# Kernel optimization log

Hardware: AMD Instinct MI355X
Metric: run time of the kernel (lower is better)

Reference implementation:

```python
import jax, jax.numpy as jnp
import numpy as np

EPS = 1e-6
B, S, D, H = 2, 1024, 1024, 16
HD = D // H


def setup_inputs() -> dict:
    key = jax.random.key(0)
    ks = jax.random.split(key, 16)
    def n(k, shape, s=1.0):
        return jax.random.normal(k, shape, dtype=jnp.float32) * s
    def u(k, shape):
        # positive scales in [0.01, 0.11)
        return jax.random.uniform(k, shape, dtype=jnp.float32) * 0.1 + 0.01
    return {
        'q_loc': n(ks[0], (B, S, D)), 'q_scale': u(ks[1], (B, S, D)),
        'k_loc': n(ks[2], (B, S, D)), 'k_scale': u(ks[3], (B, S, D)),
        'v_loc': n(ks[4], (B, S, D)), 'v_scale': u(ks[5], (B, S, D)),
        'Wq': n(ks[6], (D, D), 0.02), 'bq': n(ks[7], (D,), 0.02),
        'Wk': n(ks[8], (D, D), 0.02), 'bk': n(ks[9], (D,), 0.02),
        'Wv': n(ks[10], (D, D), 0.02), 'bv': n(ks[11], (D,), 0.02),
        'Wo': n(ks[12], (D, D), 0.02), 'bo': n(ks[13], (D,), 0.02),
        'tau': jnp.ones((), dtype=jnp.float32),
    }


def _affine(loc, scale, W, b):
    # GaussianDiag.affine: mean -> x@W^T+b ; var -> var @ (W^2)^T (diag-Gaussian linear push-through)
    new_loc = loc @ W.T + b
    new_scale = jnp.sqrt((scale * scale) @ (W * W).T)
    return new_loc, new_scale


def _split(x):  # [B,S,D] -> [B,H,S,HD]
    b, s, d = x.shape
    return x.reshape(b, s, H, d // H).transpose(0, 2, 1, 3)


def _merge(x):  # [B,H,S,HD] -> [B,S,D]
    b, h, s, hd = x.shape
    return x.transpose(0, 2, 1, 3).reshape(b, s, h * hd)


def reference(q_loc, q_scale, k_loc, k_scale, v_loc, v_scale,
              Wq, bq, Wk, bk, Wv, bv, Wo, bo, tau):
    # projections (mean and variance paths)
    qm, qs = _affine(q_loc, q_scale, Wq, bq)
    km, ks_ = _affine(k_loc, k_scale, Wk, bk)
    vm, vs = _affine(v_loc, v_scale, Wv, bv)

    qmu, kmu, vmu = _split(qm), _split(km), _split(vm)       # [B,H,S,HD]
    vvar = (_split(vs) + EPS) ** 2                           # GaussianDiag(split(loc), log(split(scale)+eps))

    # bilinear_moment: mean path matmul, variance path is constant 0.1 (+eps through log-sqrt wrap)
    score_mu = jnp.einsum('bhsd,bhtd->bhst', qmu, kmu)       # [B,H,S,S]
    score_var = jnp.float32(0.1) + EPS

    # scale by sqrt(head_dim) / head_dim
    s_mu = score_mu / np.float32(np.sqrt(HD))
    s_var = score_var / HD + EPS

    # temperature
    l_mu = s_mu / tau
    l_var = s_var / (tau * tau) + EPS                        # scalar (traced)

    # softmax_via_samples: softmax of mean, constant scale 0.01 -> var 1e-4
    top_mu = jax.nn.softmax(l_mu, axis=-1)
    top_var = jnp.float32(1e-4)

    # softmax_logit_normal (probit approximation + delta-method variance)
    adj = l_mu / jnp.sqrt(1.0 + (jnp.pi / 8.0) * l_var)
    rest_mu = jax.nn.softmax(adj, axis=-1)
    rest_var = rest_mu * (1.0 - rest_mu) * l_var

    # combine_top_rest: add means and variances (+eps through wrap)
    attn_mu = top_mu + rest_mu
    attn_var = top_var + rest_var + EPS

    # linear_combination: attn.mean @ V.mean ; attn.var @ V.var
    y_mu = jnp.einsum('bhst,bhtd->bhsd', attn_mu, vmu)
    y_var = jnp.einsum('bhst,bhtd->bhsd', attn_var, vvar)
    y_scale = jnp.sqrt(y_var + EPS)

    out_loc_pre = _merge(y_mu)
    out_scale_pre = _merge(y_scale) + EPS
    out_loc, out_scale = _affine(out_loc_pre, out_scale_pre, Wo, bo)
    return out_loc, out_scale
```

## Files before the change

### kernel.cpp

```cpp
#include <hip/hip_runtime.h>

typedef unsigned short ushort_t;
typedef __attribute__((ext_vector_type(4))) short sh4;
typedef __attribute__((ext_vector_type(8))) short short8;
typedef __attribute__((ext_vector_type(4))) float floatx4;

#define EPS 1e-6f

static __device__ __forceinline__ float b2f(ushort_t u) {
  unsigned int x = ((unsigned int)u) << 16;
  return __builtin_bit_cast(float, x);
}
static __device__ __forceinline__ ushort_t f2b(float f) {
  unsigned int u = __builtin_bit_cast(unsigned int, f);
  u = (u + 0x7FFFu + ((u >> 16) & 1u)) >> 16;
  return (ushort_t)u;
}
static __device__ __forceinline__ bool tau_is_f32(const void* taup) {
  return ((const ushort_t*)taup)[0] == 0;
}
static __device__ __forceinline__ float read_tau(const void* taup) {
  return tau_is_f32(taup) ? ((const float*)taup)[0] : b2f(((const ushort_t*)taup)[0]);
}

__global__ __launch_bounds__(256) void convert_kernel(
    const void* s0, const void* s1, const void* s2, const void* s3,
    const void* s4, const void* s5, const void* s6,
    ushort_t* __restrict__ dst, const void* taup)
{
  if (!tau_is_f32(taup)) return;
  int seg = blockIdx.y;
  const void* src; int size; int off;
  switch (seg) {
    case 0: src = s0; size = 2097152; off = 0;       break;
    case 1: src = s1; size = 2097152; off = 2097152; break;
    case 2: src = s2; size = 2097152; off = 4194304; break;
    case 3: src = s3; size = 1048576; off = 6291456; break;
    case 4: src = s4; size = 1048576; off = 7340032; break;
    case 5: src = s5; size = 1048576; off = 8388608; break;
    default: src = s6; size = 1048576; off = 9437184; break;
  }
  int i = (blockIdx.x * 256 + threadIdx.x) * 4;
  if (i >= size) return;
  ushort_t* d = dst + off + i;
  float4 v = ((const float4*)src)[i >> 2];
  d[0] = f2b(v.x); d[1] = f2b(v.y); d[2] = f2b(v.z); d[3] = f2b(v.w);
}

__global__ __launch_bounds__(256) void gemm_proj(
    const ushort_t* cA0, const ushort_t* cA1, const ushort_t* cA2,
    const ushort_t* cB0, const ushort_t* cB1, const ushort_t* cB2,
    const void* oA0, const void* oA1, const void* oA2,
    const void* oB0, const void* oB1, const void* oB2,
    const void* b0, const void* b1, const void* b2p,
    ushort_t* C0, ushort_t* C1, ushort_t* vtp,
    const void* taup)
{
  const int K = 1024, N = 1024;
  int z = blockIdx.z;
  bool f32io = tau_is_f32(taup);
  const ushort_t* A = f32io ? ((z == 0) ? cA0 : ((z == 1) ? cA1 : cA2))
                            : (const ushort_t*)((z == 0) ? oA0 : ((z == 1) ? oA1 : oA2));
  const ushort_t* B = f32io ? ((z == 0) ? cB0 : ((z == 1) ? cB1 : cB2))
                            : (const ushort_t*)((z == 0) ? oB0 : ((z == 1) ? oB1 : oB2));
  const void* bias  = (z == 0) ? b0 : ((z == 1) ? b1 : b2p);
  ushort_t* C       = (z == 0) ? C0 : C1;

  __shared__ __align__(16) ushort_t a_s[128 * 72];
  __shared__ __align__(16) ushort_t b_s[128 * 72];

  int tid = threadIdx.x;
  int lane = tid & 63, w = tid >> 6;
  int quad = lane >> 4, l16 = lane & 15;
  int m0 = blockIdx.y * 128, n0 = blockIdx.x * 128;
  int wm = (w & 1) * 64, wn = (w >> 1) * 64;

  floatx4 acc[4][4] = {};
  int srow = tid >> 3;
  int scol = (tid & 7) * 8;

  short8 pa[4], pb[4];
#pragma unroll
  for (int p = 0; p < 4; p++) {
    pa[p] = *(const short8*)(A + (size_t)(m0 + srow + p * 32) * K + scol);
    pb[p] = *(const short8*)(B + (size_t)(n0 + srow + p * 32) * K + scol);
  }

  for (int k0 = 0; k0 < K; k0 += 64) {
    __syncthreads();
#pragma unroll
    for (int p = 0; p < 4; p++) {
      *(short8*)(&a_s[(srow + p * 32) * 72 + scol]) = pa[p];
      *(short8*)(&b_s[(srow + p * 32) * 72 + scol]) = pb[p];
    }
    __syncthreads();
    if (k0 + 64 < K) {
#pragma unroll
      for (int p = 0; p < 4; p++) {
        pa[p] = *(const short8*)(A + (size_t)(m0 + srow + p * 32) * K + k0 + 64 + scol);
        pb[p] = *(const short8*)(B + (size_t)(n0 + srow + p * 32) * K + k0 + 64 + scol);
      }
    }
#pragma unroll
    for (int half = 0; half < 2; half++) {
      short8 af[4], bf[4];
#pragma unroll
      for (int i = 0; i < 4; i++)
        af[i] = *(short8*)(&a_s[(wm + i * 16 + l16) * 72 + half * 32 + quad * 8]);
#pragma unroll
      for (int j = 0; j < 4; j++)
        bf[j] = *(short8*)(&b_s[(wn + j * 16 + l16) * 72 + half * 32 + quad * 8]);
      __builtin_amdgcn_s_setprio(1);
#pragma unroll
      for (int i = 0; i < 4; i++)
#pragma unroll
        for (int j = 0; j < 4; j++)
          acc[i][j] = __builtin_amdgcn_mfma_f32_16x16x32_bf16(af[i], bf[j], acc[i][j], 0, 0, 0);
      __builtin_amdgcn_s_setprio(0);
    }
  }

  float bvv[4];
#pragma unroll
  for (int j = 0; j < 4; j++) {
    int n = n0 + wn + j * 16 + l16;
    bvv[j] = f32io ? ((const float*)bias)[n] : b2f(((const ushort_t*)bias)[n]);
  }
  if (z == 2) {
#pragma unroll
    for (int i = 0; i < 4; i++)
#pragma unroll
      for (int j = 0; j < 4; j++) {
        int n = n0 + wn + j * 16 + l16;
        int mrow = m0 + wm + i * 16 + quad * 4;
        int bb = mrow >> 10, s = mrow & 1023;
        sh4 pk4;
#pragma unroll
        for (int r = 0; r < 4; r++) pk4[r] = (short)f2b(acc[i][j][r] + bvv[j]);
        *(sh4*)(vtp + ((size_t)((bb * 16 + (n >> 6)) * 64 + (n & 63))) * 1024 + s) = pk4;
      }
  } else {
#pragma unroll
    for (int i = 0; i < 4; i++)
#pragma unroll
      for (int j = 0; j < 4; j++) {
        int n = n0 + wn + j * 16 + l16;
#pragma unroll
        for (int r = 0; r < 4; r++) {
          int m = m0 + wm + i * 16 + quad * 4 + r;
          C[(size_t)m * N + n] = f2b(acc[i][j][r] + bvv[j]);
        }
      }
  }
}

__global__ __launch_bounds__(256) void gemm_out64(
    const ushort_t* __restrict__ Abf,
    const void* __restrict__ Bv,
    const void* __restrict__ biasv,
    const ushort_t* __restrict__ Bc,
    const float* __restrict__ rsc,
    void* __restrict__ C,
    const void* taup)
{
  const int K = 1024, N = 1024;
  bool f32io = tau_is_f32(taup);
  const ushort_t* B = f32io ? Bc : (const ushort_t*)Bv;

  __shared__ __align__(16) ushort_t a_s[64 * 72];
  __shared__ __align__(16) ushort_t b_s[64 * 72];

  int tid = threadIdx.x;
  int lane = tid & 63, w = tid >> 6;
  int quad = lane >> 4, l16 = lane & 15;
  int m0 = blockIdx.y * 64, n0 = blockIdx.x * 64;
  int wm = (w & 1) * 32, wn = (w >> 1) * 32;

  floatx4 acc[2][2] = {};
  int srow = tid >> 3;
  int scol = (tid & 7) * 8;

  short8 pa[2], pb[2];
#pragma unroll
  for (int p = 0; p < 2; p++) {
    pa[p] = *(const short8*)(Abf + (size_t)(m0 + srow + p * 32) * K + scol);
    pb[p] = *(const short8*)(B + (size_t)(n0 + srow + p * 32) * K + scol);
  }

  for (int k0 = 0; k0 < K; k0 += 64) {
    __syncthreads();
#pragma unroll
    for (int p = 0; p < 2; p++) {
      *(short8*)(&a_s[(srow + p * 32) * 72 + scol]) = pa[p];
      *(short8*)(&b_s[(srow + p * 32) * 72 + scol]) = pb[p];
    }
    __syncthreads();
    if (k0 + 64 < K) {
#pragma unroll
      for (int p = 0; p < 2; p++) {
        pa[p] = *(const short8*)(Abf + (size_t)(m0 + srow + p * 32) * K + k0 + 64 + scol);
        pb[p] = *(const short8*)(B + (size_t)(n0 + srow + p * 32) * K + k0 + 64 + scol);
      }
    }
#pragma unroll
    for (int half = 0; half < 2; half++) {
      short8 af[2], bf[2];
#pragma unroll
      for (int i = 0; i < 2; i++)
        af[i] = *(short8*)(&a_s[(wm + i * 16 + l16) * 72 + half * 32 + quad * 8]);
#pragma unroll
      for (int j = 0; j < 2; j++)
        bf[j] = *(short8*)(&b_s[(wn + j * 16 + l16) * 72 + half * 32 + quad * 8]);
      __builtin_amdgcn_s_setprio(1);
#pragma unroll
      for (int i = 0; i < 2; i++)
#pragma unroll
        for (int j = 0; j < 2; j++)
          acc[i][j] = __builtin_amdgcn_mfma_f32_16x16x32_bf16(af[i], bf[j], acc[i][j], 0, 0, 0);
      __builtin_amdgcn_s_setprio(0);
    }
  }

  int b = m0 >> 10;
  float bvv[2], rsv[2];
#pragma unroll
  for (int j = 0; j < 2; j++) {
    int n = n0 + wn + j * 16 + l16;
    bvv[j] = f32io ? ((const float*)biasv)[n] : b2f(((const ushort_t*)biasv)[n]);
    rsv[j] = rsc[b * 1024 + n];
  }
#pragma unroll
  for (int i = 0; i < 2; i++)
#pragma unroll
    for (int j = 0; j < 2; j++) {
      int n = n0 + wn + j * 16 + l16;
#pragma unroll
      for (int r = 0; r < 4; r++) {
        int m = m0 + wm + i * 16 + quad * 4 + r;
        float val = acc[i][j][r] + bvv[j];
        size_t idx = (size_t)m * N + n;
        if (f32io) {
          ((float*)C)[idx] = val;
          ((float*)C)[2097152 + idx] = rsv[j];
        } else {
          ((ushort_t*)C)[idx] = f2b(val);
          ((ushort_t*)C)[2097152 + idx] = f2b(rsv[j]);
        }
      }
    }
}

__global__ __launch_bounds__(256) void flash_kernel(
    const ushort_t* __restrict__ qm, const ushort_t* __restrict__ km,
    const ushort_t* __restrict__ vt, const void* taup,
    ushort_t* __restrict__ ymu)
{
  const int S = 1024, D = 1024, HD = 64;
  int bh = blockIdx.x; int b = bh >> 4, h = bh & 15;
  int q0 = blockIdx.y * 64;
  int tid = threadIdx.x, lane = tid & 63, w = tid >> 6, quad = lane >> 4, l16 = lane & 15;
  float tau = read_tau(taup);
  float scl2 = 1.44269504f / (8.0f * tau);

  __shared__ __align__(16) ushort_t k_s[64 * 72];
  __shared__ __align__(16) ushort_t v_s[64 * 72];
  __shared__ __align__(16) ushort_t p_s[4][16 * 72];

  const ushort_t* qbase = qm + ((size_t)(b * S + q0 + w * 16 + l16)) * D + h * HD;
  short8 qa0 = *(const short8*)(qbase + quad * 8);
  short8 qa1 = *(const short8*)(qbase + 32 + quad * 8);

  floatx4 O[4] = {};
  float lrow = 0.f;

  int srow = tid >> 3;
  int scol = (tid & 7) * 8;

  short8 pk[2], pv[2];
#pragma unroll
  for (int p = 0; p < 2; p++) {
    int rr = srow + p * 32;
    pk[p] = *(const short8*)(km + ((size_t)(b * S + rr)) * D + h * HD + scol);
    pv[p] = *(const short8*)(vt + ((size_t)(bh * 64 + rr)) * 1024 + scol);
  }

  for (int t0 = 0; t0 < S; t0 += 64) {
    __syncthreads();
#pragma unroll
    for (int p = 0; p < 2; p++) {
      int rr = srow + p * 32;
      *(short8*)(&k_s[rr * 72 + scol]) = pk[p];
      *(short8*)(&v_s[rr * 72 + scol]) = pv[p];
    }
    __syncthreads();
    if (t0 + 64 < S) {
#pragma unroll
      for (int p = 0; p < 2; p++) {
        int rr = srow + p * 32;
        pk[p] = *(const short8*)(km + ((size_t)(b * S + t0 + 64 + rr)) * D + h * HD + scol);
        pv[p] = *(const short8*)(vt + ((size_t)(bh * 64 + rr)) * 1024 + t0 + 64 + scol);
      }
    }

    floatx4 Sacc[4];
    __builtin_amdgcn_s_setprio(1);
#pragma unroll
    for (int j = 0; j < 4; j++) {
      short8 kb0 = *(short8*)(&k_s[(j * 16 + l16) * 72 + quad * 8]);
      short8 kb1 = *(short8*)(&k_s[(j * 16 + l16) * 72 + 32 + quad * 8]);
      floatx4 zz = {0.f, 0.f, 0.f, 0.f};
      zz = __builtin_amdgcn_mfma_f32_16x16x32_bf16(kb0, qa0, zz, 0, 0, 0);
      zz = __builtin_amdgcn_mfma_f32_16x16x32_bf16(kb1, qa1, zz, 0, 0, 0);
      Sacc[j] = zz;
    }
    __builtin_amdgcn_s_setprio(0);

    float ls = 0.f;
#pragma unroll
    for (int j = 0; j < 4; j++) {
      float e0 = exp2f(Sacc[j][0] * scl2);
      float e1 = exp2f(Sacc[j][1] * scl2);
      float e2 = exp2f(Sacc[j][2] * scl2);
      float e3 = exp2f(Sacc[j][3] * scl2);
      ls += (e0 + e1) + (e2 + e3);
      unsigned int u01 = (unsigned int)f2b(e0) | ((unsigned int)f2b(e1) << 16);
      unsigned int u23 = (unsigned int)f2b(e2) | ((unsigned int)f2b(e3) << 16);
      *(unsigned int*)(&p_s[w][l16 * 72 + j * 16 + quad * 4]) = u01;
      *(unsigned int*)(&p_s[w][l16 * 72 + j * 16 + quad * 4 + 2]) = u23;
    }
    lrow += ls;
    __builtin_amdgcn_sched_barrier(0);
    short8 pa0 = *(short8*)(&p_s[w][l16 * 72 + quad * 8]);
    short8 pa1 = *(short8*)(&p_s[w][l16 * 72 + 32 + quad * 8]);

    __builtin_amdgcn_s_setprio(1);
#pragma unroll
    for (int jt = 0; jt < 4; jt++) {
      short8 vb0 = *(short8*)(&v_s[(jt * 16 + l16) * 72 + quad * 8]);
      short8 vb1 = *(short8*)(&v_s[(jt * 16 + l16) * 72 + 32 + quad * 8]);
      O[jt] = __builtin_amdgcn_mfma_f32_16x16x32_bf16(pa0, vb0, O[jt], 0, 0, 0);
      O[jt] = __builtin_amdgcn_mfma_f32_16x16x32_bf16(pa1, vb1, O[jt], 0, 0, 0);
    }
    __builtin_amdgcn_s_setprio(0);
  }

  lrow += __shfl_xor(lrow, 16, 64);
  lrow += __shfl_xor(lrow, 32, 64);

#pragma unroll
  for (int r = 0; r < 4; r++) {
    float lr = __shfl(lrow, quad * 4 + r, 64);
    float inv = 2.0f / lr;
    size_t mg = (size_t)(b * S + q0 + w * 16 + quad * 4 + r) * D + h * HD;
#pragma unroll
    for (int jt = 0; jt < 4; jt++)
      ymu[mg + jt * 16 + l16] = f2b(O[jt][r] * inv);
  }
}

__global__ __launch_bounds__(256) void zero_kernel(float* __restrict__ p) {
  p[blockIdx.x * 256 + threadIdx.x] = 0.0f;
}

__global__ __launch_bounds__(256) void colsum_sq_kernel(
    const void* __restrict__ vsc, const void* taup, float* __restrict__ Sx)
{
  int b = blockIdx.x, jg = blockIdx.y, sg = blockIdx.z;
  int c = threadIdx.x & 63, p = threadIdx.x >> 6;
  int j = jg * 64 + c;
  bool f32 = tau_is_f32(taup);
  size_t base = (size_t)b * 1048576 + j + (size_t)(sg * 64 + p * 16) * 1024;
  float acc = 0.f;
#pragma unroll
  for (int s = 0; s < 16; s++) {
    size_t idx = base + (size_t)s * 1024;
    float v = f32 ? ((const float*)vsc)[idx] : b2f(((const ushort_t*)vsc)[idx]);
    acc += v * v;
  }
  __shared__ float red[256];
  red[threadIdx.x] = acc;
  __syncthreads();
  if (p == 0)
    atomicAdd(&Sx[b * 1024 + j], red[c] + red[c + 64] + red[c + 128] + red[c + 192]);
}

__global__ __launch_bounds__(256) void gemv_sq_kernel(
    const float* __restrict__ x, const void* __restrict__ Wnat,
    const void* taup, float* __restrict__ out, int mode)
{
  bool f32io = tau_is_f32(taup);
  int row = blockIdx.x * 4 + (threadIdx.x >> 6);
  int lane = threadIdx.x & 63;
  int b = row >> 10, i = row & 1023;
  const float* xr = x + b * 1024 + lane * 16;
  float acc = 0.f;
  if (f32io) {
    const float* Wr = (const float*)Wnat + (size_t)i * 1024 + lane * 16;
#pragma unroll
    for (int e = 0; e < 16; e += 4) {
      float4 wv = *(const float4*)(Wr + e);
      acc += wv.x * wv.x * xr[e] + wv.y * wv.y * xr[e + 1]
           + wv.z * wv.z * xr[e + 2] + wv.w * wv.w * xr[e + 3];
    }
  } else {
    const ushort_t* Wr = (const ushort_t*)Wnat + (size_t)i * 1024 + lane * 16;
#pragma unroll
    for (int hh = 0; hh < 2; hh++) {
      short8 wv = *(const short8*)(Wr + hh * 8);
#pragma unroll
      for (int e = 0; e < 8; e++) {
        float wf = b2f((ushort_t)wv[e]);
        acc += wf * wf * xr[hh * 8 + e];
      }
    }
  }
#pragma unroll
  for (int d = 1; d < 64; d <<= 1) acc += __shfl_xor(acc, d, 64);
  if (lane == 0) {
    float r;
    if (mode == 0) {
      float tau = read_tau(taup);
      float s_var = (0.1f + EPS) / 64.0f + EPS;
      float l_var = s_var / (tau * tau) + EPS;
      float cc = (1e-4f + EPS) + l_var * (1.0f / 1024.0f);
      float ys = sqrtf(cc * acc + EPS) + EPS;
      r = ys * ys;
    } else {
      r = sqrtf(acc);
    }
    out[row] = r;
  }
}

extern "C" void kernel_launch(void* const* d_in, const int* in_sizes, int n_in,
                              void* d_out, int out_size, void* d_ws, size_t ws_size,
                              hipStream_t stream)
{
  const void* q_loc   = d_in[0];
  const void* k_loc   = d_in[2];
  const void* v_loc   = d_in[4];
  const void* v_scale = d_in[5];
  const void* Wq = d_in[6];
  const void* bq = d_in[7];
  const void* Wk = d_in[8];
  const void* bk = d_in[9];
  const void* Wv = d_in[10];
  const void* bv = d_in[11];
  const void* Wo = d_in[12];
  const void* bo = d_in[13];
  const void* tau = d_in[14];

  char* ws = (char*)d_ws;
  ushort_t* conv = (ushort_t*)ws;
  ushort_t* cq  = conv;
  ushort_t* ck  = conv + 2097152;
  ushort_t* cv  = conv + 4194304;
  ushort_t* cWq = conv + 6291456;
  ushort_t* cWk = conv + 7340032;
  ushort_t* cWv = conv + 8388608;
  ushort_t* cWo = conv + 9437184;
  ushort_t* qm  = (ushort_t*)(ws + 20971520);
  ushort_t* km  = (ushort_t*)(ws + 25165824);
  ushort_t* vt  = (ushort_t*)(ws + 29360128);
  ushort_t* ymu = (ushort_t*)(ws + 33554432);
  float* Sx  = (float*)(ws + 37748736);
  float* A2  = (float*)(ws + 37756928);
  float* rsc = (float*)(ws + 37765120);

  hipLaunchKernelGGL(zero_kernel, dim3(8), dim3(256), 0, stream, Sx);
  hipLaunchKernelGGL(convert_kernel, dim3(2048, 7), dim3(256), 0, stream,
                     q_loc, k_loc, v_loc, Wq, Wk, Wv, Wo, conv, tau);
  hipLaunchKernelGGL(gemm_proj, dim3(8, 16, 3), dim3(256), 0, stream,
                     cq, ck, cv, cWq, cWk, cWv,
                     q_loc, k_loc, v_loc, Wq, Wk, Wv,
                     bq, bk, bv, qm, km, vt, tau);
  hipLaunchKernelGGL(colsum_sq_kernel, dim3(2, 16, 16), dim3(256), 0, stream, v_scale, tau, Sx);
  hipLaunchKernelGGL(gemv_sq_kernel, dim3(512), dim3(256), 0, stream, Sx, Wv, tau, A2, 0);
  hipLaunchKernelGGL(gemv_sq_kernel, dim3(512), dim3(256), 0, stream, A2, Wo, tau, rsc, 1);
  hipLaunchKernelGGL(flash_kernel, dim3(32, 16), dim3(256), 0, stream, qm, km, vt, tau, ymu);
  hipLaunchKernelGGL(gemm_out64, dim3(16, 32), dim3(256), 0, stream,
                     ymu, Wo, bo, cWo, rsc, d_out, tau);
}
```

Before: 196.3 us.

## Double-buffer flash K/V tiles, shrink projection GEMM tiles, fold zeroing into convert

The flash attention kernel now double-buffers the K and V tiles in shared memory. It stores the prefetched next tile after the PV MFMAs, so each iteration needs only one barrier instead of two. The projection GEMM drops from 128x128 to 128x64 output tiles, doubling the grid so the 3x16x8 launch fills more CUs, at the cost of less operand reuse per block. The separate zero kernel launch is removed and its zeroing is folded into the convert kernel.

```diff
diff --git a/kernel.cpp b/kernel.cpp
--- a/kernel.cpp
+++ b/kernel.cpp
@@ -26,8 +26,10 @@
 __global__ __launch_bounds__(256) void convert_kernel(
     const void* s0, const void* s1, const void* s2, const void* s3,
     const void* s4, const void* s5, const void* s6,
-    ushort_t* __restrict__ dst, const void* taup)
-{
+    ushort_t* __restrict__ dst, const void* taup, float* __restrict__ Sx)
+{
+  if (blockIdx.y == 0 && blockIdx.x < 8)
+    Sx[blockIdx.x * 256 + threadIdx.x] = 0.0f;
   if (!tau_is_f32(taup)) return;
   int seg = blockIdx.y;
   const void* src; int size; int off;
@@ -67,62 +69,65 @@
   ushort_t* C       = (z == 0) ? C0 : C1;
 
   __shared__ __align__(16) ushort_t a_s[128 * 72];
-  __shared__ __align__(16) ushort_t b_s[128 * 72];
+  __shared__ __align__(16) ushort_t b_s[64 * 72];
 
   int tid = threadIdx.x;
   int lane = tid & 63, w = tid >> 6;
   int quad = lane >> 4, l16 = lane & 15;
-  int m0 = blockIdx.y * 128, n0 = blockIdx.x * 128;
-  int wm = (w & 1) * 64, wn = (w >> 1) * 64;
-
-  floatx4 acc[4][4] = {};
+  int m0 = blockIdx.y * 128, n0 = blockIdx.x * 64;
+  int wm = (w & 1) * 64, wn = (w >> 1) * 32;
+
+  floatx4 acc[4][2] = {};
   int srow = tid >> 3;
   int scol = (tid & 7) * 8;
 
-  short8 pa[4], pb[4];
-#pragma unroll
-  for (int p = 0; p < 4; p++) {
+  short8 pa[4], pb[2];
+#pragma unroll
+  for (int p = 0; p < 4; p++)
     pa[p] = *(const short8*)(A + (size_t)(m0 + srow + p * 32) * K + scol);
+#pragma unroll
+  for (int p = 0; p < 2; p++)
     pb[p] = *(const short8*)(B + (size_t)(n0 + srow + p * 32) * K + scol);
-  }
 
   for (int k0 = 0; k0 < K; k0 += 64) {
     __syncthreads();
 #pragma unroll
-    for (int p = 0; p < 4; p++) {
+    for (int p = 0; p < 4; p++)
       *(short8*)(&a_s[(srow + p * 32) * 72 + scol]) = pa[p];
+#pragma unroll
+    for (int p = 0; p < 2; p++)
       *(short8*)(&b_s[(srow + p * 32) * 72 + scol]) = pb[p];
-    }
     __syncthreads();
     if (k0 + 64 < K) {
 #pragma unroll
-      for (int p = 0; p < 4; p++) {
+      for (int p = 0; p < 4; p++)
         pa[p] = *(const short8*)(A + (size_t)(m0 + srow + p * 32) * K + k0 + 64 + scol);
+#pragma unroll
+      for (int p = 0; p < 2; p++)
         pb[p] = *(const short8*)(B + (size_t)(n0 + srow + p * 32) * K + k0 + 64 + scol);
-      }
     }
 #pragma unroll
     for (int half = 0; half < 2; half++) {
-      short8 af[4], bf[4];
+      short8 af[4], bf[2];
 #pragma unroll
       for (int i = 0; i < 4; i++)
         af[i] = *(short8*)(&a_s[(wm + i * 16 + l16) * 72 + half * 32 + quad * 8]);
 #pragma unroll
-      for (int j = 0; j < 4; j++)
+      for (int j = 0; j < 2; j++)
         bf[j] = *(short8*)(&b_s[(wn + j * 16 + l16) * 72 + half * 32 + quad * 8]);
       __builtin_amdgcn_s_setprio(1);
 #pragma unroll
       for (int i = 0; i < 4; i++)
 #pragma unroll
-        for (int j = 0; j < 4; j++)
+        for (int j = 0; j < 2; j++)
           acc[i][j] = __builtin_amdgcn_mfma_f32_16x16x32_bf16(af[i], bf[j], acc[i][j], 0, 0, 0);
       __builtin_amdgcn_s_setprio(0);
     }
   }
 
-  float bvv[4];
-#pragma unroll
-  for (int j = 0; j < 4; j++) {
+  float bvv[2];
+#pragma unroll
+  for (int j = 0; j < 2; j++) {
     int n = n0 + wn + j * 16 + l16;
     bvv[j] = f32io ? ((const float*)bias)[n] : b2f(((const ushort_t*)bias)[n]);
   }
@@ -130,7 +135,7 @@
 #pragma unroll
     for (int i = 0; i < 4; i++)
 #pragma unroll
-      for (int j = 0; j < 4; j++) {
+      for (int j = 0; j < 2; j++) {
         int n = n0 + wn + j * 16 + l16;
         int mrow = m0 + wm + i * 16 + quad * 4;
         int bb = mrow >> 10, s = mrow & 1023;
@@ -143,7 +148,7 @@
 #pragma unroll
     for (int i = 0; i < 4; i++)
 #pragma unroll
-      for (int j = 0; j < 4; j++) {
+      for (int j = 0; j < 2; j++) {
         int n = n0 + wn + j * 16 + l16;
 #pragma unroll
         for (int r = 0; r < 4; r++) {
@@ -262,8 +267,8 @@
   float tau = read_tau(taup);
   float scl2 = 1.44269504f / (8.0f * tau);
 
-  __shared__ __align__(16) ushort_t k_s[64 * 72];
-  __shared__ __align__(16) ushort_t v_s[64 * 72];
+  __shared__ __align__(16) ushort_t k_s[2 * 64 * 72];
+  __shared__ __align__(16) ushort_t v_s[2 * 64 * 72];
   __shared__ __align__(16) ushort_t p_s[4][16 * 72];
 
   const ushort_t* qbase = qm + ((size_t)(b * S + q0 + w * 16 + l16)) * D + h * HD;
@@ -283,17 +288,18 @@
     pk[p] = *(const short8*)(km + ((size_t)(b * S + rr)) * D + h * HD + scol);
     pv[p] = *(const short8*)(vt + ((size_t)(bh * 64 + rr)) * 1024 + scol);
   }
+#pragma unroll
+  for (int p = 0; p < 2; p++) {
+    int rr = srow + p * 32;
+    *(short8*)(&k_s[rr * 72 + scol]) = pk[p];
+    *(short8*)(&v_s[rr * 72 + scol]) = pv[p];
+  }
+  __syncthreads();
+  int cur = 0;
 
   for (int t0 = 0; t0 < S; t0 += 64) {
-    __syncthreads();
-#pragma unroll
-    for (int p = 0; p < 2; p++) {
-      int rr = srow + p * 32;
-      *(short8*)(&k_s[rr * 72 + scol]) = pk[p];
-      *(short8*)(&v_s[rr * 72 + scol]) = pv[p];
-    }
-    __syncthreads();
-    if (t0 + 64 < S) {
+    bool nxt = (t0 + 64 < S);
+    if (nxt) {
 #pragma unroll
       for (int p = 0; p < 2; p++) {
         int rr = srow + p * 32;
@@ -301,13 +307,14 @@
         pv[p] = *(const short8*)(vt + ((size_t)(bh * 64 + rr)) * 1024 + t0 + 64 + scol);
       }
     }
+    int cb = cur * 4608;
 
     floatx4 Sacc[4];
     __builtin_amdgcn_s_setprio(1);
 #pragma unroll
     for (int j = 0; j < 4; j++) {
-      short8 kb0 = *(short8*)(&k_s[(j * 16 + l16) * 72 + quad * 8]);
-      short8 kb1 = *(short8*)(&k_s[(j * 16 + l16) * 72 + 32 + quad * 8]);
+      short8 kb0 = *(short8*)(&k_s[cb + (j * 16 + l16) * 72 + quad * 8]);
+      short8 kb1 = *(short8*)(&k_s[cb + (j * 16 + l16) * 72 + 32 + quad * 8]);
       floatx4 zz = {0.f, 0.f, 0.f, 0.f};
       zz = __builtin_amdgcn_mfma_f32_16x16x32_bf16(kb0, qa0, zz, 0, 0, 0);
       zz = __builtin_amdgcn_mfma_f32_16x16x32_bf16(kb1, qa1, zz, 0, 0, 0);
@@ -336,12 +343,24 @@
     __builtin_amdgcn_s_setprio(1);
 #pragma unroll
     for (int jt = 0; jt < 4; jt++) {
-      short8 vb0 = *(short8*)(&v_s[(jt * 16 + l16) * 72 + quad * 8]);
-      short8 vb1 = *(short8*)(&v_s[(jt * 16 + l16) * 72 + 32 + quad * 8]);
+      short8 vb0 = *(short8*)(&v_s[cb + (jt * 16 + l16) * 72 + quad * 8]);
+      short8 vb1 = *(short8*)(&v_s[cb + (jt * 16 + l16) * 72 + 32 + quad * 8]);
       O[jt] = __builtin_amdgcn_mfma_f32_16x16x32_bf16(pa0, vb0, O[jt], 0, 0, 0);
       O[jt] = __builtin_amdgcn_mfma_f32_16x16x32_bf16(pa1, vb1, O[jt], 0, 0, 0);
     }
     __builtin_amdgcn_s_setprio(0);
+
+    if (nxt) {
+      int ob = (cur ^ 1) * 4608;
+#pragma unroll
+      for (int p = 0; p < 2; p++) {
+        int rr = srow + p * 32;
+        *(short8*)(&k_s[ob + rr * 72 + scol]) = pk[p];
+        *(short8*)(&v_s[ob + rr * 72 + scol]) = pv[p];
+      }
+    }
+    __syncthreads();
+    cur ^= 1;
   }
 
   lrow += __shfl_xor(lrow, 16, 64);
@@ -356,10 +375,6 @@
     for (int jt = 0; jt < 4; jt++)
       ymu[mg + jt * 16 + l16] = f2b(O[jt][r] * inv);
   }
-}
-
-__global__ __launch_bounds__(256) void zero_kernel(float* __restrict__ p) {
-  p[blockIdx.x * 256 + threadIdx.x] = 0.0f;
 }
 
 __global__ __launch_bounds__(256) void colsum_sq_kernel(
@@ -467,10 +482,9 @@
   float* A2  = (float*)(ws + 37756928);
   float* rsc = (float*)(ws + 37765120);
 
-  hipLaunchKernelGGL(zero_kernel, dim3(8), dim3(256), 0, stream, Sx);
   hipLaunchKernelGGL(convert_kernel, dim3(2048, 7), dim3(256), 0, stream,
-                     q_loc, k_loc, v_loc, Wq, Wk, Wv, Wo, conv, tau);
-  hipLaunchKernelGGL(gemm_proj, dim3(8, 16, 3), dim3(256), 0, stream,
+                     q_loc, k_loc, v_loc, Wq, Wk, Wv, Wo, conv, tau, Sx);
+  hipLaunchKernelGGL(gemm_proj, dim3(16, 16, 3), dim3(256), 0, stream,
                      cq, ck, cv, cWq, cWk, cWv,
                      q_loc, k_loc, v_loc, Wq, Wk, Wv,
                      bq, bk, bv, qm, km, vt, tau);
```

Result: faster. 189.6 us (-3.4%).
